# Optimization experiments

Measured on AMD Instinct MI355X. Metric: run time of the kernel, lower is better.

## Reference

```python
import jax, jax.numpy as jnp
import numpy as np

DIM = 1024
NUM_HEADS = 16
DH = DIM // NUM_HEADS  # 64
B, S = 4, 2048


def setup_inputs() -> dict:
    key = jax.random.key(0)
    ks = jax.random.split(key, 9)
    sc = 0.02
    x = jax.random.normal(ks[0], (B, S, DIM), dtype=jnp.float32)
    # per-head projection weights stacked: [H, DIM, DH] (input-major layout)
    Wq = jax.random.normal(ks[1], (NUM_HEADS, DIM, DH), dtype=jnp.float32) * sc
    Wk = jax.random.normal(ks[2], (NUM_HEADS, DIM, DH), dtype=jnp.float32) * sc
    Wv = jax.random.normal(ks[3], (NUM_HEADS, DIM, DH), dtype=jnp.float32) * sc
    bq = jax.random.normal(ks[4], (NUM_HEADS, DH), dtype=jnp.float32) * sc
    bk = jax.random.normal(ks[5], (NUM_HEADS, DH), dtype=jnp.float32) * sc
    bv = jax.random.normal(ks[6], (NUM_HEADS, DH), dtype=jnp.float32) * sc
    Wo = jax.random.normal(ks[7], (DIM, DIM), dtype=jnp.float32) * sc  # (in, out)
    bo = jax.random.normal(ks[8], (DIM,), dtype=jnp.float32) * sc
    return {"x": x, "Wq": Wq, "Wk": Wk, "Wv": Wv,
            "bq": bq, "bk": bk, "bv": bv, "Wo": Wo, "bo": bo}


def reference(x, Wq, Wk, Wv, bq, bk, bv, Wo, bo):
    # Per-head Linear projections, vectorized over heads: [B,H,S,DH]
    q = jnp.einsum('bsd,hde->bhse', x, Wq) + bq[None, :, None, :]
    k = jnp.einsum('bsd,hde->bhse', x, Wk) + bk[None, :, None, :]
    v = jnp.einsum('bsd,hde->bhse', x, Wv) + bv[None, :, None, :]
    # attention_matmul: Q @ K^T normalized by sqrt(dim_per_head)
    scale = 1.0 / jnp.sqrt(jnp.asarray(DH, dtype=x.dtype))
    scores = jnp.einsum('bhse,bhte->bhst', q, k) * scale  # [B,H,S,S]
    attn = jax.nn.softmax(scores, axis=-1)
    # attn_drop with p=0.0 is identity
    o = jnp.einsum('bhst,bhte->bhse', attn, v)  # [B,H,S,DH]
    # concat along last dim in head order -> [B,S,H*DH]
    o = jnp.transpose(o, (0, 2, 1, 3)).reshape(x.shape[0], x.shape[1], NUM_HEADS * DH)
    # output projection (proj_drop p=0.0 is identity)
    return o @ Wo + bo
```

## Files before the change

kernel.cpp:

```cpp
#include <hip/hip_runtime.h>
#include <stdint.h>

#define DIM 1024
#define NH 16
#define DH 64
#define BATCH 4
#define SEQ 2048
#define MROWS (BATCH*SEQ)

typedef _Float16 half8 __attribute__((ext_vector_type(8)));
typedef __fp16 fp16x2 __attribute__((ext_vector_type(2)));
typedef float f32x4 __attribute__((ext_vector_type(4)));
typedef float f32x16 __attribute__((ext_vector_type(16)));
typedef unsigned int u32x2 __attribute__((ext_vector_type(2)));

__device__ __forceinline__ unsigned short f2h(float f) {
    union { _Float16 h; unsigned short u; } c; c.h = (_Float16)f; return c.u;
}
__device__ __forceinline__ unsigned int pk2u(float a, float b) {
    union { fp16x2 h; unsigned int u; } c;
    c.h = __builtin_amdgcn_cvt_pkrtz(a, b);
    return c.u;
}
__device__ __forceinline__ float fexp2(float x) {
    return __builtin_amdgcn_exp2f(x);
}
__device__ __forceinline__ void gl_lds16(const unsigned short* g, unsigned short* l) {
    __builtin_amdgcn_global_load_lds(
        (__attribute__((address_space(1))) void*)(void*)g,
        (__attribute__((address_space(3))) void*)(void*)l,
        16, 0, 0);
}


__global__ void cast_x_kernel(const float* __restrict__ x,
                              unsigned short* __restrict__ xh, int n4) {
    int i = blockIdx.x * blockDim.x + threadIdx.x;
    if (i >= n4) return;
    float4 v = reinterpret_cast<const float4*>(x)[i];
    uint2 o;
    o.x = pk2u(v.x, v.y);
    o.y = pk2u(v.z, v.w);
    reinterpret_cast<uint2*>(xh)[i] = o;
}

__global__ __launch_bounds__(256) void prep_w_kernel(
    const float* __restrict__ Wq, const float* __restrict__ Wk,
    const float* __restrict__ Wv, const float* __restrict__ Wo,
    unsigned short* __restrict__ wt, unsigned short* __restrict__ wot)
{
    __shared__ unsigned short tile[64][65];
    const int d0 = blockIdx.x * 64;
    const int y = blockIdx.y;
    const int mat = blockIdx.z;
    const int c = threadIdx.x & 63;
    const int rr = threadIdx.x >> 6;

    if (mat < 3) {
        const float* W = (mat == 0) ? Wq : ((mat == 1) ? Wk : Wv);
#pragma unroll
        for (int p = 0; p < 16; p++) {
            int dl = p * 4 + rr;
            tile[dl][c] = f2h(W[((size_t)y * 1024 + d0 + dl) * 64 + c]);
        }
        __syncthreads();
#pragma unroll
        for (int p = 0; p < 16; p++) {
            int el = p * 4 + rr;
            wt[(((size_t)(mat * NH + y) * 64) + el) * DIM + d0 + c] = tile[c][el];
        }
    } else {
        const int o0 = y * 64;
#pragma unroll
        for (int p = 0; p < 16; p++) {
            int dl = p * 4 + rr;
            tile[dl][c] = f2h(Wo[(size_t)(d0 + dl) * DIM + o0 + c]);
        }
        __syncthreads();
#pragma unroll
        for (int p = 0; p < 16; p++) {
            int ol = p * 4 + rr;
            wot[(size_t)(o0 + ol) * DIM + d0 + c] = tile[c][ol];
        }
    }
}

__global__ __launch_bounds__(256) void qkv_gemm_kernel(
    const unsigned short* __restrict__ xh,
    const unsigned short* __restrict__ wt,
    const float* __restrict__ bq, const float* __restrict__ bk,
    const float* __restrict__ bv,
    unsigned short* __restrict__ Qb,
    unsigned short* __restrict__ Kb,
    unsigned short* __restrict__ Vt)
{
    const int rowblk = blockIdx.x;
    const int hpair = blockIdx.y;
    const int mat = blockIdx.z;
    const int wave = threadIdx.x >> 6;
    const int lane = threadIdx.x & 63;
    const int quad = lane >> 4;
    const int lr = lane & 15;
    const int mhalf = wave & 1;
    const int nhalf = wave >> 1;

    __shared__ __align__(16) unsigned short Ab[2][128 * 32];
    __shared__ __align__(16) unsigned short Bt[2][128 * 32];

    const unsigned short* Asrc = xh + (size_t)rowblk * 128 * DIM;
    const unsigned short* Bsrc = wt + (size_t)(mat * NH + hpair * 2) * DH * DIM;

    const int srow = lane >> 2;
    const int scs = lane & 3;

    f32x4 acc[4][4];
#pragma unroll
    for (int mt = 0; mt < 4; mt++)
#pragma unroll
        for (int nt = 0; nt < 4; nt++) acc[mt][nt] = (f32x4){0.f, 0.f, 0.f, 0.f};

    auto stage = [&](int k0, int sel) {
#pragma unroll
        for (int jj = 0; jj < 2; jj++) {
            const int j = wave * 2 + jj;
            const int r = j * 16 + srow;
            const int cg = scs ^ ((r >> 1) & 3);
            gl_lds16(Asrc + (size_t)r * DIM + k0 + cg * 8, &Ab[sel][j * 512]);
            gl_lds16(Bsrc + (size_t)r * DIM + k0 + cg * 8, &Bt[sel][j * 512]);
        }
    };

    stage(0, 0);
    __syncthreads();

    for (int i = 0; i < DIM / 32; i++) {
        const int sel = i & 1;
        if (i + 1 < DIM / 32) stage((i + 1) * 32, sel ^ 1);

        half8 af[4], bf[4];
#pragma unroll
        for (int mt = 0; mt < 4; mt++) {
            const int row = mhalf * 64 + mt * 16 + lr;
            const int slot = quad ^ ((row >> 1) & 3);
            af[mt] = *reinterpret_cast<const half8*>(&Ab[sel][row * 32 + slot * 8]);
        }
#pragma unroll
        for (int nt = 0; nt < 4; nt++) {
            const int row = nhalf * 64 + nt * 16 + lr;
            const int slot = quad ^ ((row >> 1) & 3);
            bf[nt] = *reinterpret_cast<const half8*>(&Bt[sel][row * 32 + slot * 8]);
        }
#pragma unroll
        for (int mt = 0; mt < 4; mt++)
#pragma unroll
            for (int nt = 0; nt < 4; nt++)
                acc[mt][nt] = __builtin_amdgcn_mfma_f32_16x16x32_f16(
                    af[mt], bf[nt], acc[mt][nt], 0, 0, 0);
        __syncthreads();
    }

    const float* bias = (mat == 0) ? bq : ((mat == 1) ? bk : bv);
    const float scale = (mat == 0) ? 0.1803368801111601f : 1.0f;
    const int rowBase = rowblk * 128 + mhalf * 64;
    const int bb = rowBase / SEQ;
    const int sBase = rowBase % SEQ;

    if (mat < 2) {
        unsigned short* outp = (mat == 0) ? Qb : Kb;
#pragma unroll
        for (int mt = 0; mt < 4; mt++) {
            const int s0 = sBase + mt * 16 + quad * 4;
#pragma unroll
            for (int nt = 0; nt < 4; nt++) {
                const int e = nhalf * 64 + nt * 16 + lr;
                const int head = hpair * 2 + (e >> 6);
                const int n = e & 63;
                const float bvl = bias[head * DH + n];
                const size_t base = (size_t)(bb * NH + head) * SEQ * DH;
#pragma unroll
                for (int r = 0; r < 4; r++) {
                    outp[base + (size_t)(s0 + r) * DH + n] =
                        f2h((acc[mt][nt][r] + bvl) * scale);
                }
            }
        }
    } else {
#pragma unroll
        for (int mt = 0; mt < 4; mt++) {
            const int s0 = sBase + mt * 16 + quad * 4;
#pragma unroll
            for (int nt = 0; nt < 4; nt++) {
                const int e = nhalf * 64 + nt * 16 + lr;
                const int head = hpair * 2 + (e >> 6);
                const int n = e & 63;
                const float bvl = bias[head * DH + n];
                const size_t base = (size_t)(bb * NH + head) * DH * SEQ;
                uint2 w;
                w.x = pk2u(acc[mt][nt][0] + bvl, acc[mt][nt][1] + bvl);
                w.y = pk2u(acc[mt][nt][2] + bvl, acc[mt][nt][3] + bvl);
                *reinterpret_cast<uint2*>(&Vt[base + (size_t)n * SEQ + s0]) = w;
            }
        }
    }
}

__global__ __launch_bounds__(256, 4) void attn_kernel(
    const unsigned short* __restrict__ Qb,
    const unsigned short* __restrict__ Kb,
    const unsigned short* __restrict__ Vt,
    unsigned short* __restrict__ Ob)
{
    const int h = blockIdx.y;
    const int bb = blockIdx.z;
    const int wave = threadIdx.x >> 6;
    const int lane = threadIdx.x & 63;
    const int ql = lane & 31;
    const int hi = lane >> 5;
    const int qBase = blockIdx.x * 128 + wave * 32;

    const size_t bh = (size_t)(bb * NH + h);
    const unsigned short* Qh = Qb + bh * SEQ * DH;
    const unsigned short* Kh = Kb + bh * SEQ * DH;
    const unsigned short* Vh = Vt + bh * DH * SEQ;

    __shared__ __align__(16) unsigned short Kbuf[2][64 * 64];
    __shared__ __align__(16) unsigned short Vbuf[2][64 * 64];

    const int srow = lane >> 3;
    const int scs = lane & 7;
    int koff[2], voff[2];
#pragma unroll
    for (int jj = 0; jj < 2; jj++) {
        const int r = wave * 16 + jj * 8 + srow;
        const int cg = scs ^ srow ^ ((wave * 2 + jj) & 3);
        koff[jj] = r * DH + cg * 8;
        voff[jj] = r * SEQ + cg * 8;
    }

    auto stage_k = [&](int kt, int sel) {
        const size_t base = (size_t)kt * 64 * DH;
        gl_lds16(Kh + base + koff[0], &Kbuf[sel][wave * 1024]);
        gl_lds16(Kh + base + koff[1], &Kbuf[sel][wave * 1024 + 512]);
    };
    auto stage_v = [&](int kt, int sel) {
        const size_t base = (size_t)kt * 64;
        gl_lds16(Vh + base + voff[0], &Vbuf[sel][wave * 1024]);
        gl_lds16(Vh + base + voff[1], &Vbuf[sel][wave * 1024 + 512]);
    };

    half8 qf[4];
#pragma unroll
    for (int ks = 0; ks < 4; ks++)
        qf[ks] = *reinterpret_cast<const half8*>(
            Qh + (size_t)(qBase + ql) * DH + ks * 16 + hi * 8);

    const int slotx = (ql & 7) ^ ((ql >> 3) & 3);
    int rowb[2], soff[4];
#pragma unroll
    for (int b = 0; b < 2; b++) rowb[b] = (b * 32 + ql) * 64;
#pragma unroll
    for (int ks = 0; ks < 4; ks++) soff[ks] = ((ks * 2 + hi) ^ slotx) * 8;

    f32x16 z16;
#pragma unroll
    for (int e = 0; e < 16; e++) z16[e] = 0.f;

    f32x16 o[2];
#pragma unroll
    for (int mt = 0; mt < 2; mt++) o[mt] = z16;
    float lsA = 0.f, lsB = 0.f;
    half8 pf[4];

    auto burst = [&](int sel, bool doPV) {
        f32x16 sacc[2];
        __builtin_amdgcn_s_setprio(1);
#pragma unroll
        for (int ks = 0; ks < 4; ks++) {
#pragma unroll
            for (int b = 0; b < 2; b++) {
                half8 kf = *reinterpret_cast<const half8*>(
                    &Kbuf[sel][rowb[b] + soff[ks]]);
                sacc[b] = __builtin_amdgcn_mfma_f32_32x32x16_f16(
                    kf, qf[ks], ks ? sacc[b] : z16, 0, 0, 0);
            }
            if (doPV) {
#pragma unroll
                for (int mt = 0; mt < 2; mt++) {
                    half8 vf = *reinterpret_cast<const half8*>(
                        &Vbuf[sel][rowb[mt] + soff[ks]]);
                    o[mt] = __builtin_amdgcn_mfma_f32_32x32x16_f16(
                        vf, pf[ks], o[mt], 0, 0, 0);
                }
            }
        }
        __builtin_amdgcn_s_setprio(0);

#pragma unroll
        for (int kb = 0; kb < 2; kb++) {
            unsigned int c[8];
#pragma unroll
            for (int m = 0; m < 8; m++) {
                float a = fexp2(sacc[kb][2 * m]);
                float b2 = fexp2(sacc[kb][2 * m + 1]);
                if (m & 1) lsB += a + b2; else lsA += a + b2;
                c[m] = pk2u(a, b2);
            }
#pragma unroll
            for (int ks = 0; ks < 2; ks++) {
                u32x2 w02 = __builtin_amdgcn_permlane32_swap(
                    c[4 * ks + 0], c[4 * ks + 2], false, false);
                u32x2 w13 = __builtin_amdgcn_permlane32_swap(
                    c[4 * ks + 1], c[4 * ks + 3], false, false);
                union { unsigned int u[4]; half8 h; } cv;
                cv.u[0] = w02[0]; cv.u[1] = w13[0];
                cv.u[2] = w02[1]; cv.u[3] = w13[1];
                pf[kb * 2 + ks] = cv.h;
            }
        }
    };

    stage_k(0, 0);
    __syncthreads();

    stage_k(1, 1);
    stage_v(0, 1);
    burst(0, false);
    __syncthreads();

    for (int i = 1; i < SEQ / 64; i++) {
        const int sel = i & 1;
        if (i + 1 < SEQ / 64) stage_k(i + 1, sel ^ 1);
        stage_v(i, sel ^ 1);
        burst(sel, true);
        __syncthreads();
    }

    __builtin_amdgcn_s_setprio(1);
#pragma unroll
    for (int ks = 0; ks < 4; ks++)
#pragma unroll
        for (int mt = 0; mt < 2; mt++) {
            half8 vf = *reinterpret_cast<const half8*>(
                &Vbuf[0][rowb[mt] + soff[ks]]);
            o[mt] = __builtin_amdgcn_mfma_f32_32x32x16_f16(
                vf, pf[ks], o[mt], 0, 0, 0);
        }
    __builtin_amdgcn_s_setprio(0);

    float l = lsA + lsB;
    l += __shfl_xor(l, 32);
    const float inv = 1.f / l;
    const size_t orow = (size_t)(bb * SEQ + qBase + ql) * DIM + h * DH;
#pragma unroll
    for (int mt = 0; mt < 2; mt++) {
#pragma unroll
        for (int g = 0; g < 4; g++) {
            uint2 pkd;
            pkd.x = pk2u(o[mt][4 * g + 0] * inv, o[mt][4 * g + 1] * inv);
            pkd.y = pk2u(o[mt][4 * g + 2] * inv, o[mt][4 * g + 3] * inv);
            *reinterpret_cast<uint2*>(Ob + orow + mt * 32 + 8 * g + 4 * hi) = pkd;
        }
    }
}

__global__ __launch_bounds__(256) void out_proj_kernel(
    const unsigned short* __restrict__ Ob,
    const unsigned short* __restrict__ wot,
    const float* __restrict__ bo,
    float* __restrict__ out)
{
    const int rowblk = blockIdx.x;
    const int colblk = blockIdx.y;
    const int wave = threadIdx.x >> 6;
    const int lane = threadIdx.x & 63;
    const int quad = lane >> 4;
    const int lr = lane & 15;
    const int mhalf = wave & 1;
    const int nhalf = wave >> 1;

    __shared__ __align__(16) unsigned short Ab[2][128 * 32];
    __shared__ __align__(16) unsigned short Bt[2][128 * 32];

    const unsigned short* Asrc = Ob + (size_t)rowblk * 128 * DIM;
    const unsigned short* Bsrc = wot + (size_t)colblk * 128 * DIM;

    const int srow = lane >> 2;
    const int scs = lane & 3;

    f32x4 acc[4][4];
#pragma unroll
    for (int mt = 0; mt < 4; mt++)
#pragma unroll
        for (int nt = 0; nt < 4; nt++) acc[mt][nt] = (f32x4){0.f, 0.f, 0.f, 0.f};

    auto stage = [&](int k0, int sel) {
#pragma unroll
        for (int jj = 0; jj < 2; jj++) {
            const int j = wave * 2 + jj;
            const int r = j * 16 + srow;
            const int cg = scs ^ ((r >> 1) & 3);
            gl_lds16(Asrc + (size_t)r * DIM + k0 + cg * 8, &Ab[sel][j * 512]);
            gl_lds16(Bsrc + (size_t)r * DIM + k0 + cg * 8, &Bt[sel][j * 512]);
        }
    };

    stage(0, 0);
    __syncthreads();

    for (int i = 0; i < DIM / 32; i++) {
        const int sel = i & 1;
        if (i + 1 < DIM / 32) stage((i + 1) * 32, sel ^ 1);

        half8 af[4], bf[4];
#pragma unroll
        for (int mt = 0; mt < 4; mt++) {
            const int row = mhalf * 64 + mt * 16 + lr;
            const int slot = quad ^ ((row >> 1) & 3);
            af[mt] = *reinterpret_cast<const half8*>(&Ab[sel][row * 32 + slot * 8]);
        }
#pragma unroll
        for (int nt = 0; nt < 4; nt++) {
            const int row = nhalf * 64 + nt * 16 + lr;
            const int slot = quad ^ ((row >> 1) & 3);
            bf[nt] = *reinterpret_cast<const half8*>(&Bt[sel][row * 32 + slot * 8]);
        }
#pragma unroll
        for (int mt = 0; mt < 4; mt++)
#pragma unroll
            for (int nt = 0; nt < 4; nt++)
                acc[mt][nt] = __builtin_amdgcn_mfma_f32_16x16x32_f16(
                    af[mt], bf[nt], acc[mt][nt], 0, 0, 0);
        __syncthreads();
    }

    const int rowBase = rowblk * 128 + mhalf * 64;
    const int colBase = colblk * 128 + nhalf * 64;
#pragma unroll
    for (int mt = 0; mt < 4; mt++) {
#pragma unroll
        for (int nt = 0; nt < 4; nt++) {
            const int col = colBase + nt * 16 + lr;
            const float bias = bo[col];
#pragma unroll
            for (int r = 0; r < 4; r++) {
                int row = rowBase + mt * 16 + quad * 4 + r;
                out[(size_t)row * DIM + col] = acc[mt][nt][r] + bias;
            }
        }
    }
}


extern "C" void kernel_launch(void* const* d_in, const int* in_sizes, int n_in,
                              void* d_out, int out_size, void* d_ws, size_t ws_size,
                              hipStream_t stream) {
    const float* x  = (const float*)d_in[0];
    const float* Wq = (const float*)d_in[1];
    const float* Wk = (const float*)d_in[2];
    const float* Wv = (const float*)d_in[3];
    const float* bq = (const float*)d_in[4];
    const float* bk = (const float*)d_in[5];
    const float* bv = (const float*)d_in[6];
    const float* Wo = (const float*)d_in[7];
    const float* bo = (const float*)d_in[8];
    float* out = (float*)d_out;

    unsigned short* xh  = (unsigned short*)d_ws;
    unsigned short* wt  = xh  + (size_t)MROWS * DIM;
    unsigned short* wot = wt  + (size_t)3 * NH * DH * DIM;
    unsigned short* Qb  = wot + (size_t)DIM * DIM;
    unsigned short* Kb  = Qb  + (size_t)BATCH * NH * SEQ * DH;
    unsigned short* Vt  = Kb  + (size_t)BATCH * NH * SEQ * DH;
    unsigned short* Ob  = Vt  + (size_t)BATCH * NH * SEQ * DH;

    {
        int n4 = MROWS * DIM / 4;
        cast_x_kernel<<<(n4 + 255) / 256, 256, 0, stream>>>(x, xh, n4);
    }
    prep_w_kernel<<<dim3(16, 16, 4), 256, 0, stream>>>(Wq, Wk, Wv, Wo, wt, wot);
    qkv_gemm_kernel<<<dim3(64, 8, 3), 256, 0, stream>>>(xh, wt, bq, bk, bv, Qb, Kb, Vt);
    attn_kernel<<<dim3(SEQ / 128, NH, BATCH), 256, 0, stream>>>(Qb, Kb, Vt, Ob);
    out_proj_kernel<<<dim3(64, 8), 256, 0, stream>>>(Ob, wot, bo, out);
}
```

Before: 316.4 us.

## Remap block IDs for XCD-local L2 reuse and stage V transpose through LDS

Flattens the grids of the QKV GEMM, attention and output projection kernels to 1D. Block IDs are remapped so that blocks landing on the same XCD (bid&7) share row blocks or batch-head groups, which is meant to improve L2 hit rates on the chiplet-partitioned MI355X. The V-transpose write in the QKV GEMM now goes through a padded LDS tile and is written out as coalesced 16-byte row stores instead of scattered 8-byte stores. In exchange the kernel uses a larger shared buffer and adds an extra barrier, and the remapping hard-codes the grid sizes.

Result: faster. 291.9 us (-7.7%).

```diff
diff --git a/kernel.cpp b/kernel.cpp
--- a/kernel.cpp
+++ b/kernel.cpp
@@ -94,9 +94,14 @@
     unsigned short* __restrict__ Kb,
     unsigned short* __restrict__ Vt)
 {
-    const int rowblk = blockIdx.x;
-    const int hpair = blockIdx.y;
-    const int mat = blockIdx.z;
+    const int bid = blockIdx.x;
+    const int xcd = bid & 7;
+    const int local = bid >> 3;
+    const int rowblk = xcd * 8 + local / 24;
+    const int rem = local % 24;
+    const int hpair = rem & 7;
+    const int mat = rem >> 3;
+
     const int wave = threadIdx.x >> 6;
     const int lane = threadIdx.x & 63;
     const int quad = lane >> 4;
@@ -104,8 +109,9 @@
     const int mhalf = wave & 1;
     const int nhalf = wave >> 1;
 
-    __shared__ __align__(16) unsigned short Ab[2][128 * 32];
-    __shared__ __align__(16) unsigned short Bt[2][128 * 32];
+    __shared__ __align__(16) unsigned short pool[128 * 136];
+    unsigned short* AbP = pool;
+    unsigned short* BtP = pool + 8192;
 
     const unsigned short* Asrc = xh + (size_t)rowblk * 128 * DIM;
     const unsigned short* Bsrc = wt + (size_t)(mat * NH + hpair * 2) * DH * DIM;
@@ -125,8 +131,8 @@
             const int j = wave * 2 + jj;
             const int r = j * 16 + srow;
             const int cg = scs ^ ((r >> 1) & 3);
-            gl_lds16(Asrc + (size_t)r * DIM + k0 + cg * 8, &Ab[sel][j * 512]);
-            gl_lds16(Bsrc + (size_t)r * DIM + k0 + cg * 8, &Bt[sel][j * 512]);
+            gl_lds16(Asrc + (size_t)r * DIM + k0 + cg * 8, AbP + sel * 4096 + j * 512);
+            gl_lds16(Bsrc + (size_t)r * DIM + k0 + cg * 8, BtP + sel * 4096 + j * 512);
         }
     };
 
@@ -142,13 +148,13 @@
         for (int mt = 0; mt < 4; mt++) {
             const int row = mhalf * 64 + mt * 16 + lr;
             const int slot = quad ^ ((row >> 1) & 3);
-            af[mt] = *reinterpret_cast<const half8*>(&Ab[sel][row * 32 + slot * 8]);
+            af[mt] = *reinterpret_cast<const half8*>(AbP + sel * 4096 + row * 32 + slot * 8);
         }
 #pragma unroll
         for (int nt = 0; nt < 4; nt++) {
             const int row = nhalf * 64 + nt * 16 + lr;
             const int slot = quad ^ ((row >> 1) & 3);
-            bf[nt] = *reinterpret_cast<const half8*>(&Bt[sel][row * 32 + slot * 8]);
+            bf[nt] = *reinterpret_cast<const half8*>(BtP + sel * 4096 + row * 32 + slot * 8);
         }
 #pragma unroll
         for (int mt = 0; mt < 4; mt++)
@@ -187,19 +193,33 @@
     } else {
 #pragma unroll
         for (int mt = 0; mt < 4; mt++) {
-            const int s0 = sBase + mt * 16 + quad * 4;
+            const int s0l = mhalf * 64 + mt * 16 + quad * 4;
 #pragma unroll
             for (int nt = 0; nt < 4; nt++) {
-                const int e = nhalf * 64 + nt * 16 + lr;
-                const int head = hpair * 2 + (e >> 6);
-                const int n = e & 63;
+                const int el = nhalf * 64 + nt * 16 + lr;
+                const int head = hpair * 2 + (el >> 6);
+                const int n = el & 63;
                 const float bvl = bias[head * DH + n];
-                const size_t base = (size_t)(bb * NH + head) * DH * SEQ;
                 uint2 w;
                 w.x = pk2u(acc[mt][nt][0] + bvl, acc[mt][nt][1] + bvl);
                 w.y = pk2u(acc[mt][nt][2] + bvl, acc[mt][nt][3] + bvl);
-                *reinterpret_cast<uint2*>(&Vt[base + (size_t)n * SEQ + s0]) = w;
-            }
+                *reinterpret_cast<uint2*>(pool + el * 136 + s0l) = w;
+            }
+        }
+        __syncthreads();
+        const int blkRow = rowblk * 128;
+        const int vb = blkRow / SEQ;
+        const int s0b = blkRow % SEQ;
+        const int sc = threadIdx.x & 15;
+        const int esub = threadIdx.x >> 4;
+#pragma unroll
+        for (int p = 0; p < 8; p++) {
+            const int el = p * 16 + esub;
+            const int head = hpair * 2 + (el >> 6);
+            const int n = el & 63;
+            uint4 v = *reinterpret_cast<const uint4*>(pool + el * 136 + sc * 8);
+            const size_t base = (size_t)(vb * NH + head) * DH * SEQ;
+            *reinterpret_cast<uint4*>(&Vt[base + (size_t)n * SEQ + s0b + sc * 8]) = v;
         }
     }
 }
@@ -210,13 +230,19 @@
     const unsigned short* __restrict__ Vt,
     unsigned short* __restrict__ Ob)
 {
-    const int h = blockIdx.y;
-    const int bb = blockIdx.z;
+    const int bid = blockIdx.x;
+    const int xcd = bid & 7;
+    const int local = bid >> 3;
+    const int bhg = xcd * 8 + (local >> 4);
+    const int qblk = local & 15;
+    const int h = bhg & 15;
+    const int bb = bhg >> 4;
+
     const int wave = threadIdx.x >> 6;
     const int lane = threadIdx.x & 63;
     const int ql = lane & 31;
     const int hi = lane >> 5;
-    const int qBase = blockIdx.x * 128 + wave * 32;
+    const int qBase = qblk * 128 + wave * 32;
 
     const size_t bh = (size_t)(bb * NH + h);
     const unsigned short* Qh = Qb + bh * SEQ * DH;
@@ -369,8 +395,12 @@
     const float* __restrict__ bo,
     float* __restrict__ out)
 {
-    const int rowblk = blockIdx.x;
-    const int colblk = blockIdx.y;
+    const int bid = blockIdx.x;
+    const int xcd = bid & 7;
+    const int local = bid >> 3;
+    const int rowblk = xcd * 8 + (local >> 3);
+    const int colblk = local & 7;
+
     const int wave = threadIdx.x >> 6;
     const int lane = threadIdx.x & 63;
     const int quad = lane >> 4;
@@ -478,7 +508,7 @@
         cast_x_kernel<<<(n4 + 255) / 256, 256, 0, stream>>>(x, xh, n4);
     }
     prep_w_kernel<<<dim3(16, 16, 4), 256, 0, stream>>>(Wq, Wk, Wv, Wo, wt, wot);
-    qkv_gemm_kernel<<<dim3(64, 8, 3), 256, 0, stream>>>(xh, wt, bq, bk, bv, Qb, Kb, Vt);
-    attn_kernel<<<dim3(SEQ / 128, NH, BATCH), 256, 0, stream>>>(Qb, Kb, Vt, Ob);
-    out_proj_kernel<<<dim3(64, 8), 256, 0, stream>>>(Ob, wot, bo, out);
-}
+    qkv_gemm_kernel<<<1536, 256, 0, stream>>>(xh, wt, bq, bk, bv, Qb, Kb, Vt);
+    attn_kernel<<<1024, 256, 0, stream>>>(Qb, Kb, Vt, Ob);
+    out_proj_kernel<<<512, 256, 0, stream>>>(Ob, wot, bo, out);
+}
```
